# Optimization experiments

Hardware: AMD Instinct MI355X
Metric: run time of the kernel (lower is better)

## Reference

```python
import jax, jax.numpy as jnp
import numpy as np

MAX_LENGTH = 4  # torch.randint(1, max_length) -> lengths in 1..MAX_LENGTH-1
MAX_WIDTH = 4
C, COLS, ROWS = 3, 3072, 3072
NUM_CRACKS = 64


def setup_inputs() -> dict:
    key = jax.random.key(0)
    k1, k2, k3, k4, k5 = jax.random.split(key, 5)
    inp = jax.random.normal(k1, (C, COLS, ROWS), dtype=jnp.float32)
    xs = jax.random.randint(k2, (2, NUM_CRACKS), 0, ROWS)
    ys = jax.random.randint(k3, (2, NUM_CRACKS), 0, COLS)
    length = jax.random.randint(k4, (NUM_CRACKS,), 1, MAX_LENGTH)
    width = jax.random.randint(k5, (NUM_CRACKS,), 1, MAX_WIDTH)
    return {
        "inp": inp,
        "x_start": xs[0], "x_end": xs[1],
        "y_start": ys[0], "y_end": ys[1],
        "length": length, "width": width,
    }


def _rasterize_mask(x_start, x_end, y_start, y_end, length, width, cols, rows):
    """Vectorized Bresenham over all cracks; returns bool mask [cols, rows]."""
    dx = jnp.abs(x_end - x_start)
    dy = jnp.abs(y_end - y_start)
    sx = jnp.where(x_start < x_end, 1, -1)
    sy = jnp.where(y_start < y_end, 1, -1)
    err0 = dx - dy
    max_steps = cols + rows  # static upper bound: steps <= dx + dy

    def step(carry, _):
        x, y, err, done = carry
        active = ~done  # loop condition held -> this pixel gets painted
        e2 = 2 * err
        cx = e2 > -dy
        cy = e2 < dx
        err_n = err - jnp.where(cx, dy, 0) + jnp.where(cy, dx, 0)
        x_n = x + jnp.where(cx, sx, 0)
        y_n = y + jnp.where(cy, sy, 0)
        x_n = jnp.where(active, x_n, x)
        y_n = jnp.where(active, y_n, y)
        err_n = jnp.where(active, err_n, err)
        done_n = done | ((x_n == x_end) & (y_n == y_end))
        return (x_n, y_n, err_n, done_n), (x, y, active)

    done0 = (x_start == x_end) & (y_start == y_end)
    _, (xs, ys, act) = jax.lax.scan(
        step, (x_start, y_start, err0, done0), None, length=max_steps)
    # xs, ys, act: [max_steps, num_cracks]; paint rectangle [y:y+width, x:x+length]
    flat = jnp.zeros(cols * rows + 1, dtype=jnp.bool_)  # last slot = drop bin
    for dw in range(MAX_WIDTH - 1):
        for dl in range(MAX_LENGTH - 1):
            yy = ys + dw
            xx = xs + dl
            valid = act & (dw < width) & (dl < length) & (yy < cols) & (xx < rows)
            idx = jnp.where(valid, yy * rows + xx, cols * rows)
            flat = flat.at[idx.ravel()].max(valid.ravel())
    return flat[:-1].reshape(cols, rows)


def reference(inp, x_start, x_end, y_start, y_end, length, width):
    cols, rows = inp.shape[-2], inp.shape[-1]
    mask = _rasterize_mask(x_start, x_end, y_start, y_end, length, width, cols, rows)
    val = inp.max()
    return jnp.where(mask[None, :, :], val, inp)
```

## Files before the change

### kernel.cpp

```cpp
#include <hip/hip_runtime.h>

#define N_COLS 3072
#define N_ROWS 3072
#define N_CH   3
#define NPIX   (N_COLS * N_ROWS)
#define NTOT   (N_CH * NPIX)
#define RED_BLOCKS  1024
#define RED_THREADS 256
#define PAINT_THREADS 256
#define PAINT_CHUNKS  12

__global__ __launch_bounds__(RED_THREADS)
void copy_max_kernel(const float* __restrict__ in, float* __restrict__ out,
                     float* __restrict__ partial) {
    const float4* in4  = (const float4*)in;
    float4*       out4 = (float4*)out;
    const int n4 = NTOT / 4;
    float m = -INFINITY;
    for (int i = blockIdx.x * blockDim.x + threadIdx.x; i < n4;
         i += gridDim.x * blockDim.x) {
        float4 v = in4[i];
        out4[i] = v;
        m = fmaxf(m, fmaxf(fmaxf(v.x, v.y), fmaxf(v.z, v.w)));
    }
    #pragma unroll
    for (int off = 32; off > 0; off >>= 1)
        m = fmaxf(m, __shfl_down(m, off, 64));
    __shared__ float smax[RED_THREADS / 64];
    const int lane = threadIdx.x & 63;
    const int wid  = threadIdx.x >> 6;
    if (lane == 0) smax[wid] = m;
    __syncthreads();
    if (threadIdx.x == 0) {
        float r = smax[0];
        #pragma unroll
        for (int w = 1; w < RED_THREADS / 64; ++w) r = fmaxf(r, smax[w]);
        partial[blockIdx.x] = r;
    }
}

__global__ __launch_bounds__(PAINT_THREADS)
void paint_kernel(const int* __restrict__ x_start, const int* __restrict__ x_end,
                  const int* __restrict__ y_start, const int* __restrict__ y_end,
                  const int* __restrict__ length,  const int* __restrict__ width,
                  float* __restrict__ out, const float* __restrict__ partial) {
    const int b  = blockIdx.y;
    const int x0 = x_start[b], x1 = x_end[b];
    const int y0 = y_start[b], y1 = y_end[b];

    if (x0 == x1 && y0 == y1) return;

    const int dx = abs(x1 - x0), dy = abs(y1 - y0);
    const int nsteps = max(dx, dy);
    if ((int)(blockIdx.x * PAINT_THREADS) >= nsteps) return;

    const int lane = threadIdx.x & 63;
    float m = -INFINITY;
    #pragma unroll
    for (int i = 0; i < RED_BLOCKS / 64; ++i) m = fmaxf(m, partial[lane + i * 64]);
    #pragma unroll
    for (int off = 32; off > 0; off >>= 1)
        m = fmaxf(m, __shfl_down(m, off, 64));
    const float val = __shfl(m, 0, 64);

    const int k = blockIdx.x * PAINT_THREADS + threadIdx.x;
    if (k >= nsteps) return;

    const int sx = (x0 < x1) ? 1 : -1;
    const int sy = (y0 < y1) ? 1 : -1;
    int X, Y;
    if (dx >= dy) {
        X = k;
        const int num = 2 * k * dy - dx;
        Y = (num <= 0) ? 0 : (num + 2 * dx - 1) / (2 * dx);
    } else {
        Y = k;
        const int num = 2 * k * dx - dy;
        X = (num <= 0) ? 0 : (num + 2 * dy - 1) / (2 * dy);
    }
    const int px = x0 + sx * X;
    const int py = y0 + sy * Y;

    const int Wv = min(width[b],  N_COLS - py);
    const int Lv = min(length[b], N_ROWS - px);
    float* chan = out + blockIdx.z * NPIX;
    for (int dw = 0; dw < Wv; ++dw) {
        const int rowp = (py + dw) * N_ROWS + px;
        for (int dl = 0; dl < Lv; ++dl)
            chan[rowp + dl] = val;
    }
}

extern "C" void kernel_launch(void* const* d_in, const int* in_sizes, int n_in,
                              void* d_out, int out_size, void* d_ws, size_t ws_size,
                              hipStream_t stream) {
    const float* inp     = (const float*)d_in[0];
    const int*   x_start = (const int*)d_in[1];
    const int*   x_end   = (const int*)d_in[2];
    const int*   y_start = (const int*)d_in[3];
    const int*   y_end   = (const int*)d_in[4];
    const int*   length  = (const int*)d_in[5];
    const int*   width   = (const int*)d_in[6];
    float*       out     = (float*)d_out;
    float*       partial = (float*)d_ws;

    copy_max_kernel<<<RED_BLOCKS, RED_THREADS, 0, stream>>>(inp, out, partial);
    dim3 pgrid(PAINT_CHUNKS, 64, N_CH);
    paint_kernel<<<pgrid, PAINT_THREADS, 0, stream>>>(
        x_start, x_end, y_start, y_end, length, width, out, partial);
}
```

Measured before the change: 46.84 us.

## Fuse copy-max and crack painting into one cooperative kernel with grid sync

```diff
diff --git a/kernel.cpp b/kernel.cpp
--- a/kernel.cpp
+++ b/kernel.cpp
@@ -1,18 +1,23 @@
 #include <hip/hip_runtime.h>
+#include <hip/hip_cooperative_groups.h>
+
+namespace cg = cooperative_groups;
 
 #define N_COLS 3072
 #define N_ROWS 3072
 #define N_CH   3
 #define NPIX   (N_COLS * N_ROWS)
 #define NTOT   (N_CH * NPIX)
-#define RED_BLOCKS  1024
-#define RED_THREADS 256
-#define PAINT_THREADS 256
-#define PAINT_CHUNKS  12
+#define BLOCKS  1024
+#define THREADS 256
+#define CHUNKS  16
 
-__global__ __launch_bounds__(RED_THREADS)
-void copy_max_kernel(const float* __restrict__ in, float* __restrict__ out,
-                     float* __restrict__ partial) {
+__global__ __launch_bounds__(THREADS)
+void fused_kernel(const float* __restrict__ in, float* __restrict__ out,
+                  float* __restrict__ partial,
+                  const int* __restrict__ x_start, const int* __restrict__ x_end,
+                  const int* __restrict__ y_start, const int* __restrict__ y_end,
+                  const int* __restrict__ length,  const int* __restrict__ width) {
     const float4* in4  = (const float4*)in;
     float4*       out4 = (float4*)out;
     const int n4 = NTOT / 4;
@@ -26,7 +31,7 @@
     #pragma unroll
     for (int off = 32; off > 0; off >>= 1)
         m = fmaxf(m, __shfl_down(m, off, 64));
-    __shared__ float smax[RED_THREADS / 64];
+    __shared__ float smax[THREADS / 64];
     const int lane = threadIdx.x & 63;
     const int wid  = threadIdx.x >> 6;
     if (lane == 0) smax[wid] = m;
@@ -34,36 +39,32 @@
     if (threadIdx.x == 0) {
         float r = smax[0];
         #pragma unroll
-        for (int w = 1; w < RED_THREADS / 64; ++w) r = fmaxf(r, smax[w]);
+        for (int w = 1; w < THREADS / 64; ++w) r = fmaxf(r, smax[w]);
         partial[blockIdx.x] = r;
     }
-}
 
-__global__ __launch_bounds__(PAINT_THREADS)
-void paint_kernel(const int* __restrict__ x_start, const int* __restrict__ x_end,
-                  const int* __restrict__ y_start, const int* __restrict__ y_end,
-                  const int* __restrict__ length,  const int* __restrict__ width,
-                  float* __restrict__ out, const float* __restrict__ partial) {
-    const int b  = blockIdx.y;
+    cg::this_grid().sync();
+
+    const int b = blockIdx.x & 63;
+    const int chunk = blockIdx.x >> 6;
+
     const int x0 = x_start[b], x1 = x_end[b];
     const int y0 = y_start[b], y1 = y_end[b];
-
     if (x0 == x1 && y0 == y1) return;
 
     const int dx = abs(x1 - x0), dy = abs(y1 - y0);
     const int nsteps = max(dx, dy);
-    if ((int)(blockIdx.x * PAINT_THREADS) >= nsteps) return;
+    if (chunk * THREADS >= nsteps) return;
 
-    const int lane = threadIdx.x & 63;
-    float m = -INFINITY;
+    float g = -INFINITY;
     #pragma unroll
-    for (int i = 0; i < RED_BLOCKS / 64; ++i) m = fmaxf(m, partial[lane + i * 64]);
+    for (int i = 0; i < BLOCKS / 64; ++i) g = fmaxf(g, partial[lane + i * 64]);
     #pragma unroll
     for (int off = 32; off > 0; off >>= 1)
-        m = fmaxf(m, __shfl_down(m, off, 64));
-    const float val = __shfl(m, 0, 64);
+        g = fmaxf(g, __shfl_down(g, off, 64));
+    const float val = __shfl(g, 0, 64);
 
-    const int k = blockIdx.x * PAINT_THREADS + threadIdx.x;
+    const int k = chunk * THREADS + threadIdx.x;
     if (k >= nsteps) return;
 
     const int sx = (x0 < x1) ? 1 : -1;
@@ -83,11 +84,13 @@
 
     const int Wv = min(width[b],  N_COLS - py);
     const int Lv = min(length[b], N_ROWS - px);
-    float* chan = out + blockIdx.z * NPIX;
     for (int dw = 0; dw < Wv; ++dw) {
         const int rowp = (py + dw) * N_ROWS + px;
-        for (int dl = 0; dl < Lv; ++dl)
-            chan[rowp + dl] = val;
+        for (int dl = 0; dl < Lv; ++dl) {
+            out[rowp + dl]            = val;
+            out[NPIX + rowp + dl]     = val;
+            out[2 * NPIX + rowp + dl] = val;
+        }
     }
 }
 
@@ -104,8 +107,10 @@
     float*       out     = (float*)d_out;
     float*       partial = (float*)d_ws;
 
-    copy_max_kernel<<<RED_BLOCKS, RED_THREADS, 0, stream>>>(inp, out, partial);
-    dim3 pgrid(PAINT_CHUNKS, 64, N_CH);
-    paint_kernel<<<pgrid, PAINT_THREADS, 0, stream>>>(
-        x_start, x_end, y_start, y_end, length, width, out, partial);
+    void* args[] = { (void*)&inp, (void*)&out, (void*)&partial,
+                     (void*)&x_start, (void*)&x_end,
+                     (void*)&y_start, (void*)&y_end,
+                     (void*)&length, (void*)&width };
+    hipLaunchCooperativeKernel((const void*)fused_kernel,
+                               dim3(BLOCKS), dim3(THREADS), args, 0, stream);
 }
```

New measurement: 151.7 us. 3.24x slower.
